# Kernel optimization log

Hardware: AMD Instinct MI355X
Metric: run time of the kernel (lower is better)

Reference implementation:

```python
import jax, jax.numpy as jnp
import numpy as np

N_NODES = 50000
N_EDGES = 800000
D_FEAT = 128
N_LAYERS = 3
HALF = 64  # units // 2 per kernel in tf_geometric MeanGraphSage
HIDDEN = 256
NUM_LABELS = 40


def setup_inputs() -> dict:
    key = jax.random.key(0)
    ks = jax.random.split(key, 6)
    x = jax.random.normal(ks[0], (N_NODES, D_FEAT), dtype=jnp.float32)
    edge_index = jax.random.randint(ks[1], (2, N_EDGES), 0, N_NODES, dtype=jnp.int32)
    self_kernels = jax.random.normal(ks[2], (N_LAYERS, D_FEAT, HALF), dtype=jnp.float32) * 0.05
    neighbor_kernels = jax.random.normal(ks[3], (N_LAYERS, D_FEAT, HALF), dtype=jnp.float32) * 0.05
    biases = jnp.zeros((N_LAYERS, 2 * HALF), dtype=jnp.float32)
    mlp_w1 = jax.random.normal(ks[4], (2 * HALF, HIDDEN), dtype=jnp.float32) * 0.05
    mlp_b1 = jnp.zeros((HIDDEN,), dtype=jnp.float32)
    mlp_w2 = jax.random.normal(ks[5], (HIDDEN, NUM_LABELS), dtype=jnp.float32) * 0.05
    mlp_b2 = jnp.zeros((NUM_LABELS,), dtype=jnp.float32)
    return {"x": x, "edge_index": edge_index, "self_kernels": self_kernels,
            "neighbor_kernels": neighbor_kernels, "biases": biases,
            "mlp_w1": mlp_w1, "mlp_b1": mlp_b1, "mlp_w2": mlp_w2, "mlp_b2": mlp_b2}


def reference(x, edge_index, self_kernels, neighbor_kernels, biases,
              mlp_w1, mlp_b1, mlp_w2, mlp_b2):
    n = x.shape[0]
    row, col = edge_index[0], edge_index[1]  # row: target node, col: source node
    # in-degree counts (graph is fixed across layers)
    ones = jnp.ones((edge_index.shape[1],), dtype=x.dtype)
    deg = jax.ops.segment_sum(ones, row, num_segments=n)  # [N]
    inv_deg = (1.0 / jnp.maximum(deg, 1.0))[:, None]      # [N,1]

    h = x
    for i in range(N_LAYERS):
        # mean-neighbor aggregation: gather source feats, segment-sum to targets
        nbr_sum = jax.ops.segment_sum(h[col], row, num_segments=n)  # [N,D]
        nbr_mean = nbr_sum * inv_deg
        from_self = h @ self_kernels[i]        # [N,HALF]
        from_nbr = nbr_mean @ neighbor_kernels[i]  # [N,HALF]
        h = jax.nn.relu(jnp.concatenate([from_self, from_nbr], axis=1) + biases[i])

    # MLP head (Flatten on [N,128] is a no-op)
    h = jax.nn.relu(h @ mlp_w1 + mlp_b1)
    return h @ mlp_w2 + mlp_b2
```

## Files before the change

### kernel.cpp

```cpp
#include <hip/hip_runtime.h>
#include <hip/hip_bf16.h>
#include <hip/hip_fp16.h>
#include <cstdint>
#include <cstddef>

#define N_NODES 50000
#define N_PAD   50176
#define N_EDGES 800000
#define D_FEAT  128
#define HALF    64
#define HIDDEN  256
#define LABELS  40

#define NBUCK 196
#define BCAP  5632
#define BUCKCAP 7424
#define EDGES_PER_BLK 4096

#define ZROW  N_PAD

#define HID_STRIDE 264

typedef __attribute__((ext_vector_type(8))) short bf16x8;
typedef __attribute__((ext_vector_type(4))) float f32x4;

#define PK_SELF(L) ((size_t)(L) * 8192)
#define PK_NBR(L)  (24576 + (size_t)(L) * 8192)
#define PK_W1      49152
#define PK_W2      81920
#define PK_TOTAL   94208

__device__ inline uint16_t f2bf_bits(float f) {
    __hip_bfloat16 b = __float2bfloat16(f);
    uint16_t u; __builtin_memcpy(&u, &b, 2); return u;
}

__device__ inline float2 h2f(uint32_t u) {
    __half2 h; __builtin_memcpy(&h, &u, 4);
    return __half22float2(h);
}

__global__ __launch_bounds__(1024) void bucket_scatter_kernel(
        const int* __restrict__ row, const int* __restrict__ col,
        int* __restrict__ bucket_cursor, uint32_t* __restrict__ staged) {
    __shared__ int hist[NBUCK];
    __shared__ int hbase[NBUCK];
    int tid  = threadIdx.x;
    int e0   = blockIdx.x * EDGES_PER_BLK;
    int eend = e0 + EDGES_PER_BLK; if (eend > N_EDGES) eend = N_EDGES;

    for (int i = tid; i < NBUCK; i += 1024) hist[i] = 0;
    __syncthreads();

    int rr[4], cc[4]; int ne = 0;
    for (int e = e0 + tid; e < eend; e += 1024) {
        rr[ne] = row[e]; cc[ne] = col[e]; ne++;
    }
    for (int i = 0; i < ne; i++) atomicAdd(&hist[rr[i] >> 8], 1);
    __syncthreads();

    for (int i = tid; i < NBUCK; i += 1024) {
        hbase[i] = atomicAdd(&bucket_cursor[i], hist[i]);
        hist[i]  = 0;
    }
    __syncthreads();

    for (int i = 0; i < ne; i++) {
        int b   = rr[i] >> 8;
        int off = atomicAdd(&hist[b], 1);
        int pos = hbase[b] + off;
        if (pos < BCAP)
            staged[(size_t)b * BCAP + pos] =
                ((uint32_t)(rr[i] & 255) << 16) | (uint32_t)cc[i];
    }
}

__global__ __launch_bounds__(1024) void bucket_fill_kernel(
        const uint32_t* __restrict__ staged, const int* __restrict__ bucket_cursor,
        int* __restrict__ deg, int* __restrict__ rowstart,
        float* __restrict__ inv_deg, int* __restrict__ csr_col) {
    __shared__ int cnt[256];
    __shared__ int excl[256];
    __shared__ int wt[4];
    __shared__ int seg[BUCKCAP];
    __shared__ int total_pad_s;
    int b   = blockIdx.x;
    int tid = threadIdx.x;

    if (tid < 256) cnt[tid] = 0;
    __syncthreads();

    int total = bucket_cursor[b]; if (total > BCAP) total = BCAP;
    const uint32_t* st = staged + (size_t)b * BCAP;

    for (int i = tid; i < total; i += 1024) atomicAdd(&cnt[st[i] >> 16], 1);
    __syncthreads();

    int lane = tid & 63, wid = tid >> 6;
    int v = 0, vp = 0, s = 0;
    if (tid < 256) {
        v  = cnt[tid];
        vp = (v + 7) & ~7;
        s  = vp;
#pragma unroll
        for (int off = 1; off < 64; off <<= 1) {
            int t = __shfl_up(s, off, 64);
            if (lane >= off) s += t;
        }
        if (lane == 63) wt[wid] = s;
    }
    __syncthreads();
    if (tid == 0) { int a = 0; for (int i = 0; i < 4; i++) { int t = wt[i]; wt[i] = a; a += t; } }
    __syncthreads();
    if (tid < 256) {
        int ex = s - vp + wt[wid];
        excl[tid] = ex;
        int node = (b << 8) + tid;
        if (node < N_NODES) {
            deg[node]      = v;
            rowstart[node] = b * BUCKCAP + ex;
            inv_deg[node]  = 1.0f / fmaxf((float)v, 1.0f);
        }
        if (tid == 255) total_pad_s = ex + vp;
        for (int q = v; q < vp; q++) seg[ex + q] = ZROW;
    }
    __syncthreads();
    for (int i = tid; i < total; i += 1024) {
        uint32_t u = st[i];
        int p = atomicAdd(&excl[u >> 16], 1);
        seg[p] = (int)(u & 0xffffu);
    }
    __syncthreads();
    int tp = total_pad_s;
    for (int i = tid; i < tp; i += 1024) csr_col[b * BUCKCAP + i] = seg[i];
}

__global__ __launch_bounds__(256) void pack_all_kernel(
        const float* __restrict__ selfk, const float* __restrict__ nbrk,
        const float* __restrict__ w1, const float* __restrict__ w2,
        __hip_bfloat16* __restrict__ wpack) {
    int m = blockIdx.y;
    const float* W; int K, Ncols, Npad; size_t dstoff;
    if (m < 3)      { W = selfk + (size_t)m*D_FEAT*HALF;      K=128; Ncols=64;  Npad=64;  dstoff = PK_SELF(m); }
    else if (m < 6) { W = nbrk  + (size_t)(m-3)*D_FEAT*HALF;  K=128; Ncols=64;  Npad=64;  dstoff = PK_NBR(m-3); }
    else if (m == 6){ W = w1;                                 K=128; Ncols=256; Npad=256; dstoff = PK_W1; }
    else            { W = w2;                                 K=256; Ncols=40;  Npad=48;  dstoff = PK_W2; }
    int ksteps = K / 32;
    int total  = ksteps * (Npad / 16) * 64;
    int t = blockIdx.x * blockDim.x + threadIdx.x;
    if (t >= total) return;
    int lane = t & 63;
    int rest = t >> 6;
    int ks   = rest % ksteps;
    int ns   = rest / ksteps;
    int colb = ns * 16 + (lane & 15);
    int kb   = ks * 32 + (lane >> 4) * 8;
    __hip_bfloat16* dst = wpack + dstoff + (size_t)t * 8;
#pragma unroll
    for (int j = 0; j < 8; j++) {
        float v = (colb < Ncols) ? W[(size_t)(kb + j) * Ncols + colb] : 0.f;
        dst[j] = __float2bfloat16(v);
    }
}

template<bool AF32>
__global__ __launch_bounds__(128, 2) void layer_gemm_kernel(
        const void* __restrict__ Ain,
        const __hip_bfloat16* __restrict__ wpack_self,
        const __hip_bfloat16* __restrict__ wpack_nbr,
        const float* __restrict__ bias,
        __hip_bfloat16* __restrict__ hout,
        uint16_t* __restrict__ zn) {
    int wave = threadIdx.x >> 6, lane = threadIdx.x & 63;
    int row0 = blockIdx.x * 64 + wave * 32;
    int lrow = lane & 15, lgrp = lane >> 4;

    const __hip_bfloat16 *hr0 = nullptr, *hr1 = nullptr;
    const float *xr0 = nullptr, *xr1 = nullptr;
    if constexpr (AF32) {
        const float* x = (const float*)Ain;
        int r0 = min(row0 + lrow, N_NODES - 1);
        int r1 = min(row0 + lrow + 16, N_NODES - 1);
        xr0 = x + (size_t)r0 * D_FEAT + lgrp * 8;
        xr1 = x + (size_t)r1 * D_FEAT + lgrp * 8;
    } else {
        const __hip_bfloat16* h = (const __hip_bfloat16*)Ain;
        hr0 = h + (size_t)(row0 + lrow) * D_FEAT + lgrp * 8;
        hr1 = hr0 + (size_t)16 * D_FEAT;
    }

    f32x4 accS[2][4] = {};
    f32x4 accN[2][4] = {};
#pragma unroll
    for (int ks = 0; ks < 4; ks++) {
        bf16x8 a0, a1;
        if constexpr (AF32) {
            float4 u0  = *(const float4*)(xr0 + ks * 32);
            float4 u0b = *(const float4*)(xr0 + ks * 32 + 4);
            float4 u1  = *(const float4*)(xr1 + ks * 32);
            float4 u1b = *(const float4*)(xr1 + ks * 32 + 4);
            float f0[8] = {u0.x, u0.y, u0.z, u0.w, u0b.x, u0b.y, u0b.z, u0b.w};
            float f1[8] = {u1.x, u1.y, u1.z, u1.w, u1b.x, u1b.y, u1b.z, u1b.w};
#pragma unroll
            for (int j = 0; j < 8; j++) { a0[j] = (short)f2bf_bits(f0[j]); a1[j] = (short)f2bf_bits(f1[j]); }
        } else {
            a0 = *(const bf16x8*)(hr0 + ks * 32);
            a1 = *(const bf16x8*)(hr1 + ks * 32);
        }
#pragma unroll
        for (int ns = 0; ns < 4; ns++) {
            bf16x8 bs = *(const bf16x8*)(wpack_self + ((size_t)(ns * 4 + ks) * 64 + lane) * 8);
            accS[0][ns] = __builtin_amdgcn_mfma_f32_16x16x32_bf16(a0, bs, accS[0][ns], 0, 0, 0);
            accS[1][ns] = __builtin_amdgcn_mfma_f32_16x16x32_bf16(a1, bs, accS[1][ns], 0, 0, 0);
            bf16x8 bn = *(const bf16x8*)(wpack_nbr + ((size_t)(ns * 4 + ks) * 64 + lane) * 8);
            accN[0][ns] = __builtin_amdgcn_mfma_f32_16x16x32_bf16(a0, bn, accN[0][ns], 0, 0, 0);
            accN[1][ns] = __builtin_amdgcn_mfma_f32_16x16x32_bf16(a1, bn, accN[1][ns], 0, 0, 0);
        }
    }
#pragma unroll
    for (int t = 0; t < 2; t++) {
#pragma unroll
        for (int ns = 0; ns < 4; ns++) {
            int colS = ns * 16 + lrow;
            float bvS = bias[colS];
#pragma unroll
            for (int i = 0; i < 4; i++) {
                int r = row0 + t * 16 + lgrp * 4 + i;
                hout[(size_t)r * D_FEAT + colS] =
                    __float2bfloat16(fmaxf(accS[t][ns][i] + bvS, 0.f));
                __half hz = __float2half(accN[t][ns][i]);
                uint16_t hb; __builtin_memcpy(&hb, &hz, 2);
                zn[(size_t)r * HALF + colS] = hb;
            }
        }
    }
}

__global__ __launch_bounds__(128) void agg8_kernel(
        const uint16_t* __restrict__ zn, const int* __restrict__ csr_col,
        const int* __restrict__ rowstart, const int* __restrict__ deg,
        const float* __restrict__ inv_deg, const float* __restrict__ bias64,
        __hip_bfloat16* __restrict__ hout) {
    int gid  = blockIdx.x * 128 + threadIdx.x;
    int wnum = gid >> 6;
    int lane = threadIdx.x & 63;
    int sub  = lane >> 3;
    int sl   = lane & 7;
    int node = wnum * 8 + sub;
    int start = __builtin_nontemporal_load(rowstart + node);
    int d     = __builtin_nontemporal_load(deg + node);
    int dpad  = (d + 7) & ~7;
    const uint32_t* zw = (const uint32_t*)zn;
    float acc[8] = {};

#define ACC8H(U) {                                                      \
    float2 t0 = h2f((U).x); acc[0] += t0.x; acc[1] += t0.y;             \
    float2 t1 = h2f((U).y); acc[2] += t1.x; acc[3] += t1.y;             \
    float2 t2 = h2f((U).z); acc[4] += t2.x; acc[5] += t2.y;             \
    float2 t3 = h2f((U).w); acc[6] += t3.x; acc[7] += t3.y; }

    if (dpad > 0) {
        int s[8];
#pragma unroll
        for (int k = 0; k < 8; k++)
            s[k] = __builtin_nontemporal_load(csr_col + start + k);
        for (int j = 0; j < dpad; j += 8) {
            int pb = min(j + 8, dpad - 8);
            int p[8];
#pragma unroll
            for (int k = 0; k < 8; k++)
                p[k] = __builtin_nontemporal_load(csr_col + start + pb + k);
            uint4 u0 = *(const uint4*)(zw + (size_t)s[0] * 32 + sl * 4);
            uint4 u1 = *(const uint4*)(zw + (size_t)s[1] * 32 + sl * 4);
            uint4 u2 = *(const uint4*)(zw + (size_t)s[2] * 32 + sl * 4);
            uint4 u3 = *(const uint4*)(zw + (size_t)s[3] * 32 + sl * 4);
            uint4 u4 = *(const uint4*)(zw + (size_t)s[4] * 32 + sl * 4);
            uint4 u5 = *(const uint4*)(zw + (size_t)s[5] * 32 + sl * 4);
            uint4 u6 = *(const uint4*)(zw + (size_t)s[6] * 32 + sl * 4);
            uint4 u7 = *(const uint4*)(zw + (size_t)s[7] * 32 + sl * 4);
            ACC8H(u0); ACC8H(u1); ACC8H(u2); ACC8H(u3);
            ACC8H(u4); ACC8H(u5); ACC8H(u6); ACC8H(u7);
#pragma unroll
            for (int k = 0; k < 8; k++) s[k] = p[k];
        }
    }
#undef ACC8H

    float inv = __builtin_nontemporal_load(inv_deg + node);
    const float* bb = bias64 + sl * 8;
    float4 b0 = *(const float4*)bb;
    float4 b1 = *(const float4*)(bb + 4);
    uint4 p;
    p.x = (uint32_t)f2bf_bits(fmaxf(acc[0] * inv + b0.x, 0.f))
        | ((uint32_t)f2bf_bits(fmaxf(acc[1] * inv + b0.y, 0.f)) << 16);
    p.y = (uint32_t)f2bf_bits(fmaxf(acc[2] * inv + b0.z, 0.f))
        | ((uint32_t)f2bf_bits(fmaxf(acc[3] * inv + b0.w, 0.f)) << 16);
    p.z = (uint32_t)f2bf_bits(fmaxf(acc[4] * inv + b1.x, 0.f))
        | ((uint32_t)f2bf_bits(fmaxf(acc[5] * inv + b1.y, 0.f)) << 16);
    p.w = (uint32_t)f2bf_bits(fmaxf(acc[6] * inv + b1.z, 0.f))
        | ((uint32_t)f2bf_bits(fmaxf(acc[7] * inv + b1.w, 0.f)) << 16);
    *(uint4*)((uint32_t*)hout + (size_t)node * 64 + 32 + sl * 4) = p;
}

__global__ __launch_bounds__(128) void mlp_fused_kernel(
        const __hip_bfloat16* __restrict__ h, const __hip_bfloat16* __restrict__ w1p,
        const float* __restrict__ b1, const __hip_bfloat16* __restrict__ w2p,
        const float* __restrict__ b2, float* __restrict__ out) {
    __shared__ __align__(16) uint16_t hid[64 * HID_STRIDE];
    int wave = threadIdx.x >> 6, lane = threadIdx.x & 63;
    int row0 = blockIdx.x * 64 + wave * 32;
    int lrow = lane & 15, lgrp = lane >> 4;

    {
        const __hip_bfloat16* ar0 = h + (size_t)(row0 + lrow) * D_FEAT + lgrp * 8;
        const __hip_bfloat16* ar1 = ar0 + (size_t)16 * D_FEAT;
        f32x4 acc[2][16] = {};
#pragma unroll 1
        for (int ks = 0; ks < 4; ks++) {
            bf16x8 a0 = *(const bf16x8*)(ar0 + ks * 32);
            bf16x8 a1 = *(const bf16x8*)(ar1 + ks * 32);
#pragma unroll
            for (int ns = 0; ns < 16; ns++) {
                bf16x8 bfr = *(const bf16x8*)(w1p + ((size_t)(ns * 4 + ks) * 64 + lane) * 8);
                acc[0][ns] = __builtin_amdgcn_mfma_f32_16x16x32_bf16(a0, bfr, acc[0][ns], 0, 0, 0);
                acc[1][ns] = __builtin_amdgcn_mfma_f32_16x16x32_bf16(a1, bfr, acc[1][ns], 0, 0, 0);
            }
        }
        int lbase = wave * 32;
#pragma unroll
        for (int t = 0; t < 2; t++) {
#pragma unroll
            for (int ns = 0; ns < 16; ns++) {
                int col = ns * 16 + lrow;
                float bv = b1[col];
#pragma unroll
                for (int i = 0; i < 4; i++) {
                    int lr = lbase + t * 16 + lgrp * 4 + i;
                    hid[lr * HID_STRIDE + col] =
                        f2bf_bits(fmaxf(acc[t][ns][i] + bv, 0.f));
                }
            }
        }
    }
    __syncthreads();

    const uint16_t* br0 = &hid[(wave * 32 + lrow) * HID_STRIDE + lgrp * 8];
    const uint16_t* br1 = br0 + 16 * HID_STRIDE;
    f32x4 acc2[2][3] = {};
#pragma unroll
    for (int ks = 0; ks < 8; ks++) {
        bf16x8 a0 = *(const bf16x8*)(br0 + ks * 32);
        bf16x8 a1 = *(const bf16x8*)(br1 + ks * 32);
#pragma unroll
        for (int ns = 0; ns < 3; ns++) {
            bf16x8 bfr = *(const bf16x8*)(w2p + ((size_t)(ns * 8 + ks) * 64 + lane) * 8);
            acc2[0][ns] = __builtin_amdgcn_mfma_f32_16x16x32_bf16(a0, bfr, acc2[0][ns], 0, 0, 0);
            acc2[1][ns] = __builtin_amdgcn_mfma_f32_16x16x32_bf16(a1, bfr, acc2[1][ns], 0, 0, 0);
        }
    }
#pragma unroll
    for (int t = 0; t < 2; t++) {
#pragma unroll
        for (int ns = 0; ns < 3; ns++) {
            int col = ns * 16 + lrow;
            if (col < LABELS) {
                float bv = b2[col];
#pragma unroll
                for (int i = 0; i < 4; i++) {
                    int r = row0 + t * 16 + lgrp * 4 + i;
                    if (r < N_NODES)
                        out[(size_t)r * LABELS + col] = acc2[t][ns][i] + bv;
                }
            }
        }
    }
}

extern "C" void kernel_launch(void* const* d_in, const int* in_sizes, int n_in,
                              void* d_out, int out_size, void* d_ws, size_t ws_size,
                              hipStream_t stream) {
    const float* x      = (const float*)d_in[0];
    const int*   ei     = (const int*)d_in[1];
    const float* selfk  = (const float*)d_in[2];
    const float* nbrk   = (const float*)d_in[3];
    const float* biases = (const float*)d_in[4];
    const float* w1     = (const float*)d_in[5];
    const float* b1     = (const float*)d_in[6];
    const float* w2     = (const float*)d_in[7];
    const float* b2     = (const float*)d_in[8];
    float* out = (float*)d_out;

    const int* row = ei;
    const int* col = ei + N_EDGES;

    char* ws = (char*)d_ws;
    size_t off = 0;
    auto alloc = [&](size_t bytes) -> char* {
        char* p = ws + off;
        off = (off + bytes + 255) & ~(size_t)255;
        return p;
    };
    int*   deg       = (int*)  alloc((size_t)N_NODES * 4);
    int*   rowstart  = (int*)  alloc((size_t)N_NODES * 4);
    float* inv_deg   = (float*)alloc((size_t)N_NODES * 4);
    int*   bucket_cursor = (int*)alloc(256 * 4);
    int*   csr_col   = (int*)  alloc((size_t)NBUCK * BUCKCAP * 4);
    uint32_t* staged = (uint32_t*)alloc((size_t)NBUCK * BCAP * 4);
    __hip_bfloat16* wpack  = (__hip_bfloat16*)alloc(PK_TOTAL * 2);
    __hip_bfloat16* hA     = (__hip_bfloat16*)alloc((size_t)N_PAD * D_FEAT * 2);
    __hip_bfloat16* hB     = (__hip_bfloat16*)alloc((size_t)N_PAD * D_FEAT * 2);
    uint16_t*       zn     = (uint16_t*)alloc((size_t)(N_PAD + 8) * HALF * 2);

    hipMemsetAsync(bucket_cursor, 0, 256 * 4, stream);
    hipMemsetAsync(zn + (size_t)ZROW * HALF, 0, HALF * 2, stream);

    const int scat_blocks = (N_EDGES + EDGES_PER_BLK - 1) / EDGES_PER_BLK;
    bucket_scatter_kernel<<<scat_blocks, 1024, 0, stream>>>(row, col, bucket_cursor, staged);
    bucket_fill_kernel<<<NBUCK, 1024, 0, stream>>>(staged, bucket_cursor,
                                                   deg, rowstart, inv_deg, csr_col);

    dim3 pgrid(16, 8);
    pack_all_kernel<<<pgrid, 256, 0, stream>>>(selfk, nbrk, w1, w2, wpack);

    const int layer_blocks = N_PAD / 64;
    const int agg_blocks   = N_NODES / 16;

    layer_gemm_kernel<true><<<layer_blocks, 128, 0, stream>>>(
        (const void*)x, wpack + PK_SELF(0), wpack + PK_NBR(0), biases, hA, zn);
    agg8_kernel<<<agg_blocks, 128, 0, stream>>>(zn, csr_col, rowstart, deg,
                                                inv_deg, biases + 64, hA);
    layer_gemm_kernel<false><<<layer_blocks, 128, 0, stream>>>(
        (const void*)hA, wpack + PK_SELF(1), wpack + PK_NBR(1), biases + 128, hB, zn);
    agg8_kernel<<<agg_blocks, 128, 0, stream>>>(zn, csr_col, rowstart, deg,
                                                inv_deg, biases + 128 + 64, hB);
    layer_gemm_kernel<false><<<layer_blocks, 128, 0, stream>>>(
        (const void*)hB, wpack + PK_SELF(2), wpack + PK_NBR(2), biases + 256, hA, zn);
    agg8_kernel<<<agg_blocks, 128, 0, stream>>>(zn, csr_col, rowstart, deg,
                                                inv_deg, biases + 256 + 64, hA);

    mlp_fused_kernel<<<layer_blocks, 128, 0, stream>>>(hA, wpack + PK_W1, b1,
                                                       wpack + PK_W2, b2, out);
}
```

Baseline: 222.5 us.

## Compress CSR indices to 16-bit, vectorize GEMM epilogue stores via swapped MFMA operands

Neighbor indices are stored as uint16 and read eight at a time with one 16-byte load, and the padded degree is precomputed so the aggregation kernel does less index traffic and arithmetic. The MFMA operands are swapped so each lane holds four consecutive output columns of one row, letting the GEMM and MLP epilogues write packed 8-byte (or float4) stores instead of scattered 2-byte stores. The GEMM and MLP blocks grow from 128 to 256 threads, covering 128 rows each. The 16-bit indices only work while node ids fit in 16 bits within a bucket, and the prefetch reads past the end of each row, which needs the extra padding added to the allocation.

Result: faster. 214.9 us (-3.4%).

```diff
diff --git a/kernel.cpp b/kernel.cpp
--- a/kernel.cpp
+++ b/kernel.cpp
@@ -33,6 +33,11 @@
 __device__ inline uint16_t f2bf_bits(float f) {
     __hip_bfloat16 b = __float2bfloat16(f);
     uint16_t u; __builtin_memcpy(&u, &b, 2); return u;
+}
+
+__device__ inline uint16_t f2h_bits(float f) {
+    __half h = __float2half(f);
+    uint16_t u; __builtin_memcpy(&u, &h, 2); return u;
 }
 
 __device__ inline float2 h2f(uint32_t u) {
@@ -77,8 +82,8 @@
 
 __global__ __launch_bounds__(1024) void bucket_fill_kernel(
         const uint32_t* __restrict__ staged, const int* __restrict__ bucket_cursor,
-        int* __restrict__ deg, int* __restrict__ rowstart,
-        float* __restrict__ inv_deg, int* __restrict__ csr_col) {
+        int* __restrict__ degpad, int* __restrict__ rowstart,
+        float* __restrict__ inv_deg, uint16_t* __restrict__ csr_col) {
     __shared__ int cnt[256];
     __shared__ int excl[256];
     __shared__ int wt[4];
@@ -117,7 +122,7 @@
         excl[tid] = ex;
         int node = (b << 8) + tid;
         if (node < N_NODES) {
-            deg[node]      = v;
+            degpad[node]   = vp;
             rowstart[node] = b * BUCKCAP + ex;
             inv_deg[node]  = 1.0f / fmaxf((float)v, 1.0f);
         }
@@ -132,7 +137,8 @@
     }
     __syncthreads();
     int tp = total_pad_s;
-    for (int i = tid; i < tp; i += 1024) csr_col[b * BUCKCAP + i] = seg[i];
+    for (int i = tid; i < tp; i += 1024)
+        csr_col[b * BUCKCAP + i] = (uint16_t)seg[i];
 }
 
 __global__ __launch_bounds__(256) void pack_all_kernel(
@@ -164,7 +170,7 @@
 }
 
 template<bool AF32>
-__global__ __launch_bounds__(128, 2) void layer_gemm_kernel(
+__global__ __launch_bounds__(256, 2) void layer_gemm_kernel(
         const void* __restrict__ Ain,
         const __hip_bfloat16* __restrict__ wpack_self,
         const __hip_bfloat16* __restrict__ wpack_nbr,
@@ -172,7 +178,7 @@
         __hip_bfloat16* __restrict__ hout,
         uint16_t* __restrict__ zn) {
     int wave = threadIdx.x >> 6, lane = threadIdx.x & 63;
-    int row0 = blockIdx.x * 64 + wave * 32;
+    int row0 = blockIdx.x * 128 + wave * 32;
     int lrow = lane & 15, lgrp = lane >> 4;
 
     const __hip_bfloat16 *hr0 = nullptr, *hr1 = nullptr;
@@ -210,35 +216,41 @@
 #pragma unroll
         for (int ns = 0; ns < 4; ns++) {
             bf16x8 bs = *(const bf16x8*)(wpack_self + ((size_t)(ns * 4 + ks) * 64 + lane) * 8);
-            accS[0][ns] = __builtin_amdgcn_mfma_f32_16x16x32_bf16(a0, bs, accS[0][ns], 0, 0, 0);
-            accS[1][ns] = __builtin_amdgcn_mfma_f32_16x16x32_bf16(a1, bs, accS[1][ns], 0, 0, 0);
+            accS[0][ns] = __builtin_amdgcn_mfma_f32_16x16x32_bf16(bs, a0, accS[0][ns], 0, 0, 0);
+            accS[1][ns] = __builtin_amdgcn_mfma_f32_16x16x32_bf16(bs, a1, accS[1][ns], 0, 0, 0);
             bf16x8 bn = *(const bf16x8*)(wpack_nbr + ((size_t)(ns * 4 + ks) * 64 + lane) * 8);
-            accN[0][ns] = __builtin_amdgcn_mfma_f32_16x16x32_bf16(a0, bn, accN[0][ns], 0, 0, 0);
-            accN[1][ns] = __builtin_amdgcn_mfma_f32_16x16x32_bf16(a1, bn, accN[1][ns], 0, 0, 0);
+            accN[0][ns] = __builtin_amdgcn_mfma_f32_16x16x32_bf16(bn, a0, accN[0][ns], 0, 0, 0);
+            accN[1][ns] = __builtin_amdgcn_mfma_f32_16x16x32_bf16(bn, a1, accN[1][ns], 0, 0, 0);
         }
     }
 #pragma unroll
     for (int t = 0; t < 2; t++) {
+        int noder = row0 + t * 16 + lrow;
+        uint16_t* hrow = (uint16_t*)hout + (size_t)noder * D_FEAT;
+        uint16_t* zrow = zn + (size_t)noder * HALF;
 #pragma unroll
         for (int ns = 0; ns < 4; ns++) {
-            int colS = ns * 16 + lrow;
-            float bvS = bias[colS];
-#pragma unroll
-            for (int i = 0; i < 4; i++) {
-                int r = row0 + t * 16 + lgrp * 4 + i;
-                hout[(size_t)r * D_FEAT + colS] =
-                    __float2bfloat16(fmaxf(accS[t][ns][i] + bvS, 0.f));
-                __half hz = __float2half(accN[t][ns][i]);
-                uint16_t hb; __builtin_memcpy(&hb, &hz, 2);
-                zn[(size_t)r * HALF + colS] = hb;
-            }
+            int c0 = ns * 16 + lgrp * 4;
+            float4 bv = *(const float4*)(bias + c0);
+            uint2 w;
+            w.x = (uint32_t)f2bf_bits(fmaxf(accS[t][ns][0] + bv.x, 0.f))
+                | ((uint32_t)f2bf_bits(fmaxf(accS[t][ns][1] + bv.y, 0.f)) << 16);
+            w.y = (uint32_t)f2bf_bits(fmaxf(accS[t][ns][2] + bv.z, 0.f))
+                | ((uint32_t)f2bf_bits(fmaxf(accS[t][ns][3] + bv.w, 0.f)) << 16);
+            *(uint2*)(hrow + c0) = w;
+            uint2 z;
+            z.x = (uint32_t)f2h_bits(accN[t][ns][0])
+                | ((uint32_t)f2h_bits(accN[t][ns][1]) << 16);
+            z.y = (uint32_t)f2h_bits(accN[t][ns][2])
+                | ((uint32_t)f2h_bits(accN[t][ns][3]) << 16);
+            *(uint2*)(zrow + c0) = z;
         }
     }
 }
 
 __global__ __launch_bounds__(128) void agg8_kernel(
-        const uint16_t* __restrict__ zn, const int* __restrict__ csr_col,
-        const int* __restrict__ rowstart, const int* __restrict__ deg,
+        const uint16_t* __restrict__ zn, const uint16_t* __restrict__ csr_col,
+        const int* __restrict__ rowstart, const int* __restrict__ degpad,
         const float* __restrict__ inv_deg, const float* __restrict__ bias64,
         __hip_bfloat16* __restrict__ hout) {
     int gid  = blockIdx.x * 128 + threadIdx.x;
@@ -247,9 +259,8 @@
     int sub  = lane >> 3;
     int sl   = lane & 7;
     int node = wnum * 8 + sub;
-    int start = __builtin_nontemporal_load(rowstart + node);
-    int d     = __builtin_nontemporal_load(deg + node);
-    int dpad  = (d + 7) & ~7;
+    int start = rowstart[node];
+    int dpad  = degpad[node];
     const uint32_t* zw = (const uint32_t*)zn;
     float acc[8] = {};
 
@@ -260,33 +271,29 @@
     float2 t3 = h2f((U).w); acc[6] += t3.x; acc[7] += t3.y; }
 
     if (dpad > 0) {
-        int s[8];
-#pragma unroll
-        for (int k = 0; k < 8; k++)
-            s[k] = __builtin_nontemporal_load(csr_col + start + k);
+        uint4 sv = *(const uint4*)(csr_col + start);
         for (int j = 0; j < dpad; j += 8) {
-            int pb = min(j + 8, dpad - 8);
-            int p[8];
-#pragma unroll
-            for (int k = 0; k < 8; k++)
-                p[k] = __builtin_nontemporal_load(csr_col + start + pb + k);
-            uint4 u0 = *(const uint4*)(zw + (size_t)s[0] * 32 + sl * 4);
-            uint4 u1 = *(const uint4*)(zw + (size_t)s[1] * 32 + sl * 4);
-            uint4 u2 = *(const uint4*)(zw + (size_t)s[2] * 32 + sl * 4);
-            uint4 u3 = *(const uint4*)(zw + (size_t)s[3] * 32 + sl * 4);
-            uint4 u4 = *(const uint4*)(zw + (size_t)s[4] * 32 + sl * 4);
-            uint4 u5 = *(const uint4*)(zw + (size_t)s[5] * 32 + sl * 4);
-            uint4 u6 = *(const uint4*)(zw + (size_t)s[6] * 32 + sl * 4);
-            uint4 u7 = *(const uint4*)(zw + (size_t)s[7] * 32 + sl * 4);
+            uint4 pv = *(const uint4*)(csr_col + start + j + 8);
+            int s0 = (int)(sv.x & 0xffffu), s1 = (int)(sv.x >> 16);
+            int s2 = (int)(sv.y & 0xffffu), s3 = (int)(sv.y >> 16);
+            int s4 = (int)(sv.z & 0xffffu), s5 = (int)(sv.z >> 16);
+            int s6 = (int)(sv.w & 0xffffu), s7 = (int)(sv.w >> 16);
+            uint4 u0 = *(const uint4*)(zw + (size_t)s0 * 32 + sl * 4);
+            uint4 u1 = *(const uint4*)(zw + (size_t)s1 * 32 + sl * 4);
+            uint4 u2 = *(const uint4*)(zw + (size_t)s2 * 32 + sl * 4);
+            uint4 u3 = *(const uint4*)(zw + (size_t)s3 * 32 + sl * 4);
+            uint4 u4 = *(const uint4*)(zw + (size_t)s4 * 32 + sl * 4);
+            uint4 u5 = *(const uint4*)(zw + (size_t)s5 * 32 + sl * 4);
+            uint4 u6 = *(const uint4*)(zw + (size_t)s6 * 32 + sl * 4);
+            uint4 u7 = *(const uint4*)(zw + (size_t)s7 * 32 + sl * 4);
             ACC8H(u0); ACC8H(u1); ACC8H(u2); ACC8H(u3);
             ACC8H(u4); ACC8H(u5); ACC8H(u6); ACC8H(u7);
-#pragma unroll
-            for (int k = 0; k < 8; k++) s[k] = p[k];
+            sv = pv;
         }
     }
 #undef ACC8H
 
-    float inv = __builtin_nontemporal_load(inv_deg + node);
+    float inv = inv_deg[node];
     const float* bb = bias64 + sl * 8;
     float4 b0 = *(const float4*)bb;
     float4 b1 = *(const float4*)(bb + 4);
@@ -302,13 +309,13 @@
     *(uint4*)((uint32_t*)hout + (size_t)node * 64 + 32 + sl * 4) = p;
 }
 
-__global__ __launch_bounds__(128) void mlp_fused_kernel(
+__global__ __launch_bounds__(256, 2) void mlp_fused_kernel(
         const __hip_bfloat16* __restrict__ h, const __hip_bfloat16* __restrict__ w1p,
         const float* __restrict__ b1, const __hip_bfloat16* __restrict__ w2p,
         const float* __restrict__ b2, float* __restrict__ out) {
-    __shared__ __align__(16) uint16_t hid[64 * HID_STRIDE];
+    __shared__ __align__(16) uint16_t hid[128 * HID_STRIDE];
     int wave = threadIdx.x >> 6, lane = threadIdx.x & 63;
-    int row0 = blockIdx.x * 64 + wave * 32;
+    int row0 = blockIdx.x * 128 + wave * 32;
     int lrow = lane & 15, lgrp = lane >> 4;
 
     {
@@ -322,23 +329,24 @@
 #pragma unroll
             for (int ns = 0; ns < 16; ns++) {
                 bf16x8 bfr = *(const bf16x8*)(w1p + ((size_t)(ns * 4 + ks) * 64 + lane) * 8);
-                acc[0][ns] = __builtin_amdgcn_mfma_f32_16x16x32_bf16(a0, bfr, acc[0][ns], 0, 0, 0);
-                acc[1][ns] = __builtin_amdgcn_mfma_f32_16x16x32_bf16(a1, bfr, acc[1][ns], 0, 0, 0);
+                acc[0][ns] = __builtin_amdgcn_mfma_f32_16x16x32_bf16(bfr, a0, acc[0][ns], 0, 0, 0);
+                acc[1][ns] = __builtin_amdgcn_mfma_f32_16x16x32_bf16(bfr, a1, acc[1][ns], 0, 0, 0);
             }
         }
         int lbase = wave * 32;
 #pragma unroll
         for (int t = 0; t < 2; t++) {
+            int lr = lbase + t * 16 + lrow;
 #pragma unroll
             for (int ns = 0; ns < 16; ns++) {
-                int col = ns * 16 + lrow;
-                float bv = b1[col];
-#pragma unroll
-                for (int i = 0; i < 4; i++) {
-                    int lr = lbase + t * 16 + lgrp * 4 + i;
-                    hid[lr * HID_STRIDE + col] =
-                        f2bf_bits(fmaxf(acc[t][ns][i] + bv, 0.f));
-                }
+                int c0 = ns * 16 + lgrp * 4;
+                float4 bv = *(const float4*)(b1 + c0);
+                uint2 w;
+                w.x = (uint32_t)f2bf_bits(fmaxf(acc[t][ns][0] + bv.x, 0.f))
+                    | ((uint32_t)f2bf_bits(fmaxf(acc[t][ns][1] + bv.y, 0.f)) << 16);
+                w.y = (uint32_t)f2bf_bits(fmaxf(acc[t][ns][2] + bv.z, 0.f))
+                    | ((uint32_t)f2bf_bits(fmaxf(acc[t][ns][3] + bv.w, 0.f)) << 16);
+                *(uint2*)&hid[lr * HID_STRIDE + c0] = w;
             }
         }
     }
@@ -354,22 +362,25 @@
 #pragma unroll
         for (int ns = 0; ns < 3; ns++) {
             bf16x8 bfr = *(const bf16x8*)(w2p + ((size_t)(ns * 8 + ks) * 64 + lane) * 8);
-            acc2[0][ns] = __builtin_amdgcn_mfma_f32_16x16x32_bf16(a0, bfr, acc2[0][ns], 0, 0, 0);
-            acc2[1][ns] = __builtin_amdgcn_mfma_f32_16x16x32_bf16(a1, bfr, acc2[1][ns], 0, 0, 0);
+            acc2[0][ns] = __builtin_amdgcn_mfma_f32_16x16x32_bf16(bfr, a0, acc2[0][ns], 0, 0, 0);
+            acc2[1][ns] = __builtin_amdgcn_mfma_f32_16x16x32_bf16(bfr, a1, acc2[1][ns], 0, 0, 0);
         }
     }
 #pragma unroll
     for (int t = 0; t < 2; t++) {
-#pragma unroll
-        for (int ns = 0; ns < 3; ns++) {
-            int col = ns * 16 + lrow;
-            if (col < LABELS) {
-                float bv = b2[col];
-#pragma unroll
-                for (int i = 0; i < 4; i++) {
-                    int r = row0 + t * 16 + lgrp * 4 + i;
-                    if (r < N_NODES)
-                        out[(size_t)r * LABELS + col] = acc2[t][ns][i] + bv;
+        int noder = row0 + t * 16 + lrow;
+        if (noder < N_NODES) {
+#pragma unroll
+            for (int ns = 0; ns < 3; ns++) {
+                int c0 = ns * 16 + lgrp * 4;
+                if (c0 < LABELS) {
+                    float4 bv = *(const float4*)(b2 + c0);
+                    float4 o;
+                    o.x = acc2[t][ns][0] + bv.x;
+                    o.y = acc2[t][ns][1] + bv.y;
+                    o.z = acc2[t][ns][2] + bv.z;
+                    o.w = acc2[t][ns][3] + bv.w;
+                    *(float4*)(out + (size_t)noder * LABELS + c0) = o;
                 }
             }
         }
@@ -400,11 +411,11 @@
         off = (off + bytes + 255) & ~(size_t)255;
         return p;
     };
-    int*   deg       = (int*)  alloc((size_t)N_NODES * 4);
+    int*   degpad    = (int*)  alloc((size_t)N_NODES * 4);
     int*   rowstart  = (int*)  alloc((size_t)N_NODES * 4);
     float* inv_deg   = (float*)alloc((size_t)N_NODES * 4);
     int*   bucket_cursor = (int*)alloc(256 * 4);
-    int*   csr_col   = (int*)  alloc((size_t)NBUCK * BUCKCAP * 4);
+    uint16_t* csr_col = (uint16_t*)alloc((size_t)NBUCK * BUCKCAP * 2 + 32);
     uint32_t* staged = (uint32_t*)alloc((size_t)NBUCK * BCAP * 4);
     __hip_bfloat16* wpack  = (__hip_bfloat16*)alloc(PK_TOTAL * 2);
     __hip_bfloat16* hA     = (__hip_bfloat16*)alloc((size_t)N_PAD * D_FEAT * 2);
@@ -417,27 +428,27 @@
     const int scat_blocks = (N_EDGES + EDGES_PER_BLK - 1) / EDGES_PER_BLK;
     bucket_scatter_kernel<<<scat_blocks, 1024, 0, stream>>>(row, col, bucket_cursor, staged);
     bucket_fill_kernel<<<NBUCK, 1024, 0, stream>>>(staged, bucket_cursor,
-                                                   deg, rowstart, inv_deg, csr_col);
+                                                   degpad, rowstart, inv_deg, csr_col);
 
     dim3 pgrid(16, 8);
     pack_all_kernel<<<pgrid, 256, 0, stream>>>(selfk, nbrk, w1, w2, wpack);
 
-    const int layer_blocks = N_PAD / 64;
+    const int layer_blocks = N_PAD / 128;
     const int agg_blocks   = N_NODES / 16;
 
-    layer_gemm_kernel<true><<<layer_blocks, 128, 0, stream>>>(
+    layer_gemm_kernel<true><<<layer_blocks, 256, 0, stream>>>(
         (const void*)x, wpack + PK_SELF(0), wpack + PK_NBR(0), biases, hA, zn);
-    agg8_kernel<<<agg_blocks, 128, 0, stream>>>(zn, csr_col, rowstart, deg,
+    agg8_kernel<<<agg_blocks, 128, 0, stream>>>(zn, csr_col, rowstart, degpad,
                                                 inv_deg, biases + 64, hA);
-    layer_gemm_kernel<false><<<layer_blocks, 128, 0, stream>>>(
+    layer_gemm_kernel<false><<<layer_blocks, 256, 0, stream>>>(
         (const void*)hA, wpack + PK_SELF(1), wpack + PK_NBR(1), biases + 128, hB, zn);
-    agg8_kernel<<<agg_blocks, 128, 0, stream>>>(zn, csr_col, rowstart, deg,
+    agg8_kernel<<<agg_blocks, 128, 0, stream>>>(zn, csr_col, rowstart, degpad,
                                                 inv_deg, biases + 128 + 64, hB);
-    layer_gemm_kernel<false><<<layer_blocks, 128, 0, stream>>>(
+    layer_gemm_kernel<false><<<layer_blocks, 256, 0, stream>>>(
         (const void*)hB, wpack + PK_SELF(2), wpack + PK_NBR(2), biases + 256, hA, zn);
-    agg8_kernel<<<agg_blocks, 128, 0, stream>>>(zn, csr_col, rowstart, deg,
+    agg8_kernel<<<agg_blocks, 128, 0, stream>>>(zn, csr_col, rowstart, degpad,
                                                 inv_deg, biases + 256 + 64, hA);
 
-    mlp_fused_kernel<<<layer_blocks, 128, 0, stream>>>(hA, wpack + PK_W1, b1,
+    mlp_fused_kernel<<<layer_blocks, 256, 0, stream>>>(hA, wpack + PK_W1, b1,
                                                        wpack + PK_W2, b2, out);
 }
```

## Use wave-per-node aggregation, 16-bit CSR indices, and 256-thread GEMM blocks

Applied to the files above, without the earlier changes.

The aggregation kernel moves from 8 nodes per wave (one 8-lane group per node, walking the whole neighbour list) to one node per wave. Its 8 lane groups each take one neighbour slot, and the partial sums are combined with an xor-shuffle reduction. The aim is to spread high-degree nodes across more lanes and balance work better, at the cost of idle lanes for low-degree nodes and extra shuffle work. CSR column indices shrink to uint16 (bucket-local node offsets) and the padded degree is precomputed, which reduces index traffic. The GEMM and MLP kernels double their block size to 256 threads, covering 128 rows per block.

Result: slower. 235.4 us (+5.8%).

```diff
diff --git a/kernel.cpp b/kernel.cpp
--- a/kernel.cpp
+++ b/kernel.cpp
@@ -77,8 +77,8 @@
 
 __global__ __launch_bounds__(1024) void bucket_fill_kernel(
         const uint32_t* __restrict__ staged, const int* __restrict__ bucket_cursor,
-        int* __restrict__ deg, int* __restrict__ rowstart,
-        float* __restrict__ inv_deg, int* __restrict__ csr_col) {
+        int* __restrict__ degpad, int* __restrict__ rowstart,
+        float* __restrict__ inv_deg, uint16_t* __restrict__ csr_col) {
     __shared__ int cnt[256];
     __shared__ int excl[256];
     __shared__ int wt[4];
@@ -117,7 +117,7 @@
         excl[tid] = ex;
         int node = (b << 8) + tid;
         if (node < N_NODES) {
-            deg[node]      = v;
+            degpad[node]   = vp;
             rowstart[node] = b * BUCKCAP + ex;
             inv_deg[node]  = 1.0f / fmaxf((float)v, 1.0f);
         }
@@ -132,7 +132,8 @@
     }
     __syncthreads();
     int tp = total_pad_s;
-    for (int i = tid; i < tp; i += 1024) csr_col[b * BUCKCAP + i] = seg[i];
+    for (int i = tid; i < tp; i += 1024)
+        csr_col[b * BUCKCAP + i] = (uint16_t)seg[i];
 }
 
 __global__ __launch_bounds__(256) void pack_all_kernel(
@@ -164,7 +165,7 @@
 }
 
 template<bool AF32>
-__global__ __launch_bounds__(128, 2) void layer_gemm_kernel(
+__global__ __launch_bounds__(256, 2) void layer_gemm_kernel(
         const void* __restrict__ Ain,
         const __hip_bfloat16* __restrict__ wpack_self,
         const __hip_bfloat16* __restrict__ wpack_nbr,
@@ -172,7 +173,7 @@
         __hip_bfloat16* __restrict__ hout,
         uint16_t* __restrict__ zn) {
     int wave = threadIdx.x >> 6, lane = threadIdx.x & 63;
-    int row0 = blockIdx.x * 64 + wave * 32;
+    int row0 = blockIdx.x * 128 + wave * 32;
     int lrow = lane & 15, lgrp = lane >> 4;
 
     const __hip_bfloat16 *hr0 = nullptr, *hr1 = nullptr;
@@ -236,20 +237,18 @@
     }
 }
 
-__global__ __launch_bounds__(128) void agg8_kernel(
-        const uint16_t* __restrict__ zn, const int* __restrict__ csr_col,
-        const int* __restrict__ rowstart, const int* __restrict__ deg,
+__global__ __launch_bounds__(256) void aggw_kernel(
+        const uint16_t* __restrict__ zn, const uint16_t* __restrict__ csr_col,
+        const int* __restrict__ rowstart, const int* __restrict__ degpad,
         const float* __restrict__ inv_deg, const float* __restrict__ bias64,
         __hip_bfloat16* __restrict__ hout) {
-    int gid  = blockIdx.x * 128 + threadIdx.x;
-    int wnum = gid >> 6;
+    int wave = threadIdx.x >> 6;
     int lane = threadIdx.x & 63;
-    int sub  = lane >> 3;
+    int node = blockIdx.x * 4 + wave;
+    int slot = lane >> 3;
     int sl   = lane & 7;
-    int node = wnum * 8 + sub;
-    int start = __builtin_nontemporal_load(rowstart + node);
-    int d     = __builtin_nontemporal_load(deg + node);
-    int dpad  = (d + 7) & ~7;
+    int start = rowstart[node];
+    int dpad  = degpad[node];
     const uint32_t* zw = (const uint32_t*)zn;
     float acc[8] = {};
 
@@ -260,33 +259,26 @@
     float2 t3 = h2f((U).w); acc[6] += t3.x; acc[7] += t3.y; }
 
     if (dpad > 0) {
-        int s[8];
-#pragma unroll
-        for (int k = 0; k < 8; k++)
-            s[k] = __builtin_nontemporal_load(csr_col + start + k);
-        for (int j = 0; j < dpad; j += 8) {
-            int pb = min(j + 8, dpad - 8);
-            int p[8];
-#pragma unroll
-            for (int k = 0; k < 8; k++)
-                p[k] = __builtin_nontemporal_load(csr_col + start + pb + k);
-            uint4 u0 = *(const uint4*)(zw + (size_t)s[0] * 32 + sl * 4);
-            uint4 u1 = *(const uint4*)(zw + (size_t)s[1] * 32 + sl * 4);
-            uint4 u2 = *(const uint4*)(zw + (size_t)s[2] * 32 + sl * 4);
-            uint4 u3 = *(const uint4*)(zw + (size_t)s[3] * 32 + sl * 4);
-            uint4 u4 = *(const uint4*)(zw + (size_t)s[4] * 32 + sl * 4);
-            uint4 u5 = *(const uint4*)(zw + (size_t)s[5] * 32 + sl * 4);
-            uint4 u6 = *(const uint4*)(zw + (size_t)s[6] * 32 + sl * 4);
-            uint4 u7 = *(const uint4*)(zw + (size_t)s[7] * 32 + sl * 4);
-            ACC8H(u0); ACC8H(u1); ACC8H(u2); ACC8H(u3);
-            ACC8H(u4); ACC8H(u5); ACC8H(u6); ACC8H(u7);
-#pragma unroll
-            for (int k = 0; k < 8; k++) s[k] = p[k];
-        }
+        int src = (int)csr_col[start + slot];
+        uint4 u = *(const uint4*)(zw + (size_t)src * 32 + sl * 4);
+        for (int j = 8; j < dpad; j += 8) {
+            int nsrc = (int)csr_col[start + j + slot];
+            uint4 v = *(const uint4*)(zw + (size_t)nsrc * 32 + sl * 4);
+            ACC8H(u);
+            u = v;
+        }
+        ACC8H(u);
     }
 #undef ACC8H
 
-    float inv = __builtin_nontemporal_load(inv_deg + node);
+#pragma unroll
+    for (int mask = 8; mask <= 32; mask <<= 1) {
+#pragma unroll
+        for (int i = 0; i < 8; i++)
+            acc[i] += __shfl_xor(acc[i], mask, 64);
+    }
+
+    float inv = inv_deg[node];
     const float* bb = bias64 + sl * 8;
     float4 b0 = *(const float4*)bb;
     float4 b1 = *(const float4*)(bb + 4);
@@ -299,16 +291,18 @@
         | ((uint32_t)f2bf_bits(fmaxf(acc[5] * inv + b1.y, 0.f)) << 16);
     p.w = (uint32_t)f2bf_bits(fmaxf(acc[6] * inv + b1.z, 0.f))
         | ((uint32_t)f2bf_bits(fmaxf(acc[7] * inv + b1.w, 0.f)) << 16);
-    *(uint4*)((uint32_t*)hout + (size_t)node * 64 + 32 + sl * 4) = p;
-}
-
-__global__ __launch_bounds__(128) void mlp_fused_kernel(
+    if (lane < 8) {
+        *(uint4*)((uint32_t*)hout + (size_t)node * 64 + 32 + lane * 4) = p;
+    }
+}
+
+__global__ __launch_bounds__(256, 2) void mlp_fused_kernel(
         const __hip_bfloat16* __restrict__ h, const __hip_bfloat16* __restrict__ w1p,
         const float* __restrict__ b1, const __hip_bfloat16* __restrict__ w2p,
         const float* __restrict__ b2, float* __restrict__ out) {
-    __shared__ __align__(16) uint16_t hid[64 * HID_STRIDE];
+    __shared__ __align__(16) uint16_t hid[128 * HID_STRIDE];
     int wave = threadIdx.x >> 6, lane = threadIdx.x & 63;
-    int row0 = blockIdx.x * 64 + wave * 32;
+    int row0 = blockIdx.x * 128 + wave * 32;
     int lrow = lane & 15, lgrp = lane >> 4;
 
     {
@@ -400,11 +394,11 @@
         off = (off + bytes + 255) & ~(size_t)255;
         return p;
     };
-    int*   deg       = (int*)  alloc((size_t)N_NODES * 4);
+    int*   degpad    = (int*)  alloc((size_t)N_NODES * 4);
     int*   rowstart  = (int*)  alloc((size_t)N_NODES * 4);
     float* inv_deg   = (float*)alloc((size_t)N_NODES * 4);
     int*   bucket_cursor = (int*)alloc(256 * 4);
-    int*   csr_col   = (int*)  alloc((size_t)NBUCK * BUCKCAP * 4);
+    uint16_t* csr_col = (uint16_t*)alloc((size_t)NBUCK * BUCKCAP * 2 + 32);
     uint32_t* staged = (uint32_t*)alloc((size_t)NBUCK * BCAP * 4);
     __hip_bfloat16* wpack  = (__hip_bfloat16*)alloc(PK_TOTAL * 2);
     __hip_bfloat16* hA     = (__hip_bfloat16*)alloc((size_t)N_PAD * D_FEAT * 2);
@@ -417,27 +411,27 @@
     const int scat_blocks = (N_EDGES + EDGES_PER_BLK - 1) / EDGES_PER_BLK;
     bucket_scatter_kernel<<<scat_blocks, 1024, 0, stream>>>(row, col, bucket_cursor, staged);
     bucket_fill_kernel<<<NBUCK, 1024, 0, stream>>>(staged, bucket_cursor,
-                                                   deg, rowstart, inv_deg, csr_col);
+                                                   degpad, rowstart, inv_deg, csr_col);
 
     dim3 pgrid(16, 8);
     pack_all_kernel<<<pgrid, 256, 0, stream>>>(selfk, nbrk, w1, w2, wpack);
 
-    const int layer_blocks = N_PAD / 64;
-    const int agg_blocks   = N_NODES / 16;
-
-    layer_gemm_kernel<true><<<layer_blocks, 128, 0, stream>>>(
+    const int layer_blocks = N_PAD / 128;
+    const int agg_blocks   = N_NODES / 4;
+
+    layer_gemm_kernel<true><<<layer_blocks, 256, 0, stream>>>(
         (const void*)x, wpack + PK_SELF(0), wpack + PK_NBR(0), biases, hA, zn);
-    agg8_kernel<<<agg_blocks, 128, 0, stream>>>(zn, csr_col, rowstart, deg,
+    aggw_kernel<<<agg_blocks, 256, 0, stream>>>(zn, csr_col, rowstart, degpad,
                                                 inv_deg, biases + 64, hA);
-    layer_gemm_kernel<false><<<layer_blocks, 128, 0, stream>>>(
+    layer_gemm_kernel<false><<<layer_blocks, 256, 0, stream>>>(
         (const void*)hA, wpack + PK_SELF(1), wpack + PK_NBR(1), biases + 128, hB, zn);
-    agg8_kernel<<<agg_blocks, 128, 0, stream>>>(zn, csr_col, rowstart, deg,
+    aggw_kernel<<<agg_blocks, 256, 0, stream>>>(zn, csr_col, rowstart, degpad,
                                                 inv_deg, biases + 128 + 64, hB);
-    layer_gemm_kernel<false><<<layer_blocks, 128, 0, stream>>>(
+    layer_gemm_kernel<false><<<layer_blocks, 256, 0, stream>>>(
         (const void*)hB, wpack + PK_SELF(2), wpack + PK_NBR(2), biases + 256, hA, zn);
-    agg8_kernel<<<agg_blocks, 128, 0, stream>>>(zn, csr_col, rowstart, deg,
+    aggw_kernel<<<agg_blocks, 256, 0, stream>>>(zn, csr_col, rowstart, degpad,
                                                 inv_deg, biases + 256 + 64, hA);
 
-    mlp_fused_kernel<<<layer_blocks, 128, 0, stream>>>(hA, wpack + PK_W1, b1,
+    mlp_fused_kernel<<<layer_blocks, 256, 0, stream>>>(hA, wpack + PK_W1, b1,
                                                        wpack + PK_W2, b2, out);
 }
```
